# Kernel tuning notes

Hardware: AMD Instinct MI355X
Metric: run time of the kernel (lower is better)

Reference implementation:

```python
import jax, jax.numpy as jnp
import numpy as np

D = 128
N_SRC = 50000
N_DST = 50000
E = 640000
NEG_SLOPE = 0.01  # torch LeakyReLU default


def _lrelu(x):
    return jax.nn.leaky_relu(x, NEG_SLOPE)


def setup_inputs() -> dict:
    key = jax.random.key(0)
    ks = jax.random.split(key, 12)
    s = 1.0 / np.sqrt(D)
    return {
        "feat_src": jax.random.normal(ks[0], (N_SRC, D), jnp.float32),
        "feat_dst": jax.random.normal(ks[1], (N_DST, D), jnp.float32),
        "src_idx": jax.random.randint(ks[2], (E,), 0, N_SRC, jnp.int32),
        "dst_idx": jax.random.randint(ks[3], (E,), 0, N_DST, jnp.int32),
        "W_src": jax.random.uniform(ks[4], (D, D), jnp.float32, -s, s),
        "b_src": jnp.zeros((D,), jnp.float32),
        "W_dst": jax.random.uniform(ks[5], (D, D), jnp.float32, -s, s),
        "b_dst": jnp.zeros((D,), jnp.float32),
        "W_a1": jax.random.uniform(ks[6], (D, D), jnp.float32, -s, s),
        "b_a1": jnp.zeros((D,), jnp.float32),
        "W_a2": jax.random.uniform(ks[7], (D, 1), jnp.float32, -s, s),
        "b_a2": jnp.zeros((1,), jnp.float32),
        "W_out": jax.random.uniform(ks[8], (D, D), jnp.float32, -s, s),
        "b_out": jnp.zeros((D,), jnp.float32),
    }


def reference(feat_src, feat_dst, src_idx, dst_idx,
              W_src, b_src, W_dst, b_dst,
              W_a1, b_a1, W_a2, b_a2, W_out, b_out):
    n_dst = feat_dst.shape[0]
    # node projections (dropout is identity in eval mode)
    hs = feat_src @ W_src + b_src            # [n_src, d]
    hd = feat_dst @ W_dst + b_dst            # [n_dst, d]
    # u_add_v: per-edge feature
    e = hs[src_idx] + hd[dst_idx]            # [E, d]
    # attention MLP: LeakyReLU -> Linear -> LeakyReLU -> Linear(d->1)
    s = _lrelu(_lrelu(e) @ W_a1 + b_a1) @ W_a2 + b_a2  # [E, 1]
    s = s[:, 0]
    # edge softmax grouped by destination node (numerically stable)
    m = jax.ops.segment_max(s, dst_idx, num_segments=n_dst)
    ex = jnp.exp(s - m[dst_idx])
    denom = jax.ops.segment_sum(ex, dst_idx, num_segments=n_dst)
    alpha = ex / denom[dst_idx]              # [E]
    # scale messages and scatter-sum to dst nodes
    n_f = jax.ops.segment_sum(alpha[:, None] * e, dst_idx, num_segments=n_dst)
    return _lrelu(n_f @ W_out + b_out)       # [n_dst, d]
```

## Files before the change

kernel.cpp:

```cpp
#include <hip/hip_runtime.h>
#include <math.h>

#define DD 128
#define NEG 0.01f
#define SCHUNK 4096

typedef __attribute__((ext_vector_type(8))) _Float16 half8;
typedef __attribute__((ext_vector_type(4))) float f32x4;

__device__ __forceinline__ float lrelu(float x){ return x > 0.f ? x : NEG * x; }

__device__ __forceinline__ unsigned short h2u(_Float16 h){
    union { _Float16 h; unsigned short u; } v; v.h = h; return v.u;
}
__device__ __forceinline__ _Float16 u2h(unsigned short u){
    union { unsigned short u; _Float16 h; } v; v.u = u; return v.h;
}

__device__ __forceinline__ half8 h8max(half8 x, half8 y){
#if __has_builtin(__builtin_elementwise_max)
    return __builtin_elementwise_max(x, y);
#else
    half8 r;
    #pragma unroll
    for (int i = 0; i < 8; i++) r[i] = x[i] > y[i] ? x[i] : y[i];
    return r;
#endif
}

__global__ void hist_pack(const int* dst, int* deg, int E, int nhist,
                          const float* Wa1, const float* Wsrc,
                          const float* Wdst, const float* Wout,
                          unsigned short* wpack){
    const int bid = blockIdx.x;
    if (bid < nhist){
        int i = bid * 256 + threadIdx.x;
        if (i < E) atomicAdd(&deg[dst[i]], 1);
    } else {
        int i = (bid - nhist) * 256 + threadIdx.x;
        if (i >= 4 * 16384) return;
        int seg = i >> 14, t = i & 16383;
        int j = t & 7, lane = (t >> 3) & 63, nt = (t >> 9) & 7, kc = t >> 12;
        int k = kc * 32 + (lane >> 4) * 8 + j;
        int n = nt * 16 + (lane & 15);
        const float* W = (seg == 0) ? Wa1 : (seg == 1) ? Wsrc : (seg == 2) ? Wdst : Wout;
        wpack[i] = h2u((_Float16)W[k * DD + n]);
    }
}

__global__ __launch_bounds__(1024) void scan1(const int* deg, int* part, int n){
    __shared__ int wsum[16];
    const int tid = threadIdx.x;
    const int lane = tid & 63, wid = tid >> 6;
    int i4 = blockIdx.x * SCHUNK + tid * 4;
    int4 v = make_int4(0, 0, 0, 0);
    if (i4 + 3 < n) v = *(const int4*)(deg + i4);
    else {
        if (i4 + 0 < n) v.x = deg[i4 + 0];
        if (i4 + 1 < n) v.y = deg[i4 + 1];
        if (i4 + 2 < n) v.z = deg[i4 + 2];
        if (i4 + 3 < n) v.w = deg[i4 + 3];
    }
    int t = v.x + v.y + v.z + v.w;
    #pragma unroll
    for (int off = 1; off < 64; off <<= 1) t += __shfl_xor(t, off, 64);
    if (lane == 0) wsum[wid] = t;
    __syncthreads();
    if (tid == 0){
        int s = 0;
        #pragma unroll
        for (int j = 0; j < 16; j++) s += wsum[j];
        part[blockIdx.x] = s;
    }
}

__global__ __launch_bounds__(1024) void scan2(const int* deg, const int* part,
        int* row_off, int* cursor, int n, int nchunks){
    __shared__ int wsum[16];
    const int tid = threadIdx.x;
    const int lane = tid & 63, wid = tid >> 6;
    const int b = blockIdx.x;
    int carry = 0;
    for (int j = 0; j < b; j++) carry += part[j];
    int i4 = b * SCHUNK + tid * 4;
    int4 v = make_int4(0, 0, 0, 0);
    if (i4 + 3 < n) v = *(const int4*)(deg + i4);
    else {
        if (i4 + 0 < n) v.x = deg[i4 + 0];
        if (i4 + 1 < n) v.y = deg[i4 + 1];
        if (i4 + 2 < n) v.z = deg[i4 + 2];
        if (i4 + 3 < n) v.w = deg[i4 + 3];
    }
    int tsum = v.x + v.y + v.z + v.w;
    int x = tsum;
    #pragma unroll
    for (int off = 1; off < 64; off <<= 1){
        int t = __shfl_up(x, off, 64);
        if (lane >= off) x += t;
    }
    if (lane == 63) wsum[wid] = x;
    __syncthreads();
    int wprefix = 0;
    #pragma unroll
    for (int j = 0; j < 16; j++) if (j < wid) wprefix += wsum[j];
    int excl = carry + wprefix + (x - tsum);
    if (i4 + 3 < n){
        int4 o;
        o.x = excl; o.y = excl + v.x; o.z = o.y + v.y; o.w = o.z + v.z;
        *(int4*)(row_off + i4) = o;
        *(int4*)(cursor + i4) = o;
    } else {
        int a = excl;
        if (i4 + 0 < n){ row_off[i4 + 0] = a; cursor[i4 + 0] = a; a += v.x; }
        if (i4 + 1 < n){ row_off[i4 + 1] = a; cursor[i4 + 1] = a; a += v.y; }
        if (i4 + 2 < n){ row_off[i4 + 2] = a; cursor[i4 + 2] = a; a += v.z; }
        if (i4 + 3 < n){ row_off[i4 + 3] = a; cursor[i4 + 3] = a; }
    }
    if (b == 0 && tid == 0){
        int tot = 0;
        for (int j = 0; j < nchunks; j++) tot += part[j];
        row_off[n] = tot;
    }
}

__global__ void scatter_pairs(const int* src, const int* dst, int* cursor,
                              int2* pairs, int* s_srcs, int E){
    int i = blockIdx.x * blockDim.x + threadIdx.x;
    if (i < E){
        int d = dst[i];
        int s = src[i];
        int pos = atomicAdd(&cursor[d], 1);
        pairs[pos] = make_int2(s, d);
        s_srcs[pos] = s;
    }
}

__global__ __launch_bounds__(256) void lin2_mfma(
        const float* X1, const unsigned short* W1, const float* b1,
        unsigned short* Yb1, int n1, int g1,
        const float* X2, const unsigned short* W2, const float* b2,
        unsigned short* Yb2, int n2){
    __shared__ unsigned short sB[16384];
    const int tid = threadIdx.x;
    const int second = (blockIdx.x >= g1);
    const float* X = second ? X2 : X1;
    const unsigned short* W = second ? W2 : W1;
    const float* b = second ? b2 : b1;
    unsigned short* Yb = second ? Yb2 : Yb1;
    const int nrows = second ? n2 : n1;
    const int bidx = second ? (blockIdx.x - g1) : blockIdx.x;
    {
        const uint4* g = (const uint4*)W;
        uint4* l = (uint4*)sB;
        #pragma unroll
        for (int t = 0; t < 8; t++) l[tid + 256 * t] = g[tid + 256 * t];
    }
    const int wave = tid >> 6, lane = tid & 63;
    const int qd = lane >> 4, ln16 = lane & 15;
    const int row0 = bidx * 128 + wave * 32;
    int r0 = row0 + ln16;       if (r0 >= nrows) r0 = nrows - 1;
    int r1 = row0 + 16 + ln16;  if (r1 >= nrows) r1 = nrows - 1;
    f32x4 acc[2][8];
    #pragma unroll
    for (int rt = 0; rt < 2; rt++)
        #pragma unroll
        for (int nt = 0; nt < 8; nt++)
            acc[rt][nt] = (f32x4){0.f, 0.f, 0.f, 0.f};
    __syncthreads();
    #pragma unroll
    for (int kc = 0; kc < 4; kc++){
        const int koff = kc * 32 + qd * 8;
        half8 a[2];
        const float* px[2] = {X + (size_t)r0 * DD + koff, X + (size_t)r1 * DD + koff};
        #pragma unroll
        for (int rt = 0; rt < 2; rt++){
            float4 v0 = *(const float4*)(px[rt]);
            float4 v1 = *(const float4*)(px[rt] + 4);
            a[rt][0] = (_Float16)v0.x; a[rt][1] = (_Float16)v0.y;
            a[rt][2] = (_Float16)v0.z; a[rt][3] = (_Float16)v0.w;
            a[rt][4] = (_Float16)v1.x; a[rt][5] = (_Float16)v1.y;
            a[rt][6] = (_Float16)v1.z; a[rt][7] = (_Float16)v1.w;
        }
        #pragma unroll
        for (int nt = 0; nt < 8; nt++){
            const int fi = (((kc << 3) + nt) << 6 | lane) << 3;
            half8 bw = *(const half8*)&sB[fi];
            acc[0][nt] = __builtin_amdgcn_mfma_f32_16x16x32_f16(a[0], bw, acc[0][nt], 0, 0, 0);
            acc[1][nt] = __builtin_amdgcn_mfma_f32_16x16x32_f16(a[1], bw, acc[1][nt], 0, 0, 0);
        }
    }
    #pragma unroll
    for (int nt = 0; nt < 8; nt++){
        const int col = nt * 16 + ln16;
        const float bv = b[col];
        #pragma unroll
        for (int rt = 0; rt < 2; rt++){
            #pragma unroll
            for (int r = 0; r < 4; r++){
                int row = row0 + rt * 16 + qd * 4 + r;
                if (row < nrows){
                    float y = acc[rt][nt][r] + bv;
                    Yb[(size_t)row * DD + col] = h2u((_Float16)y);
                }
            }
        }
    }
}

__global__ __launch_bounds__(256) void lin_mfma(const float* X,
        const unsigned short* W, const float* b, float* Y, int nrows){
    __shared__ unsigned short sB[16384];
    const int tid = threadIdx.x;
    {
        const uint4* g = (const uint4*)W;
        uint4* l = (uint4*)sB;
        #pragma unroll
        for (int t = 0; t < 8; t++) l[tid + 256 * t] = g[tid + 256 * t];
    }
    const int wave = tid >> 6, lane = tid & 63;
    const int qd = lane >> 4, ln16 = lane & 15;
    const int row0 = blockIdx.x * 128 + wave * 32;
    int r0 = row0 + ln16;       if (r0 >= nrows) r0 = nrows - 1;
    int r1 = row0 + 16 + ln16;  if (r1 >= nrows) r1 = nrows - 1;
    f32x4 acc[2][8];
    #pragma unroll
    for (int rt = 0; rt < 2; rt++)
        #pragma unroll
        for (int nt = 0; nt < 8; nt++)
            acc[rt][nt] = (f32x4){0.f, 0.f, 0.f, 0.f};
    __syncthreads();
    #pragma unroll
    for (int kc = 0; kc < 4; kc++){
        const int koff = kc * 32 + qd * 8;
        half8 a[2];
        const float* px[2] = {X + (size_t)r0 * DD + koff, X + (size_t)r1 * DD + koff};
        #pragma unroll
        for (int rt = 0; rt < 2; rt++){
            float4 v0 = *(const float4*)(px[rt]);
            float4 v1 = *(const float4*)(px[rt] + 4);
            a[rt][0] = (_Float16)v0.x; a[rt][1] = (_Float16)v0.y;
            a[rt][2] = (_Float16)v0.z; a[rt][3] = (_Float16)v0.w;
            a[rt][4] = (_Float16)v1.x; a[rt][5] = (_Float16)v1.y;
            a[rt][6] = (_Float16)v1.z; a[rt][7] = (_Float16)v1.w;
        }
        #pragma unroll
        for (int nt = 0; nt < 8; nt++){
            const int fi = (((kc << 3) + nt) << 6 | lane) << 3;
            half8 bw = *(const half8*)&sB[fi];
            acc[0][nt] = __builtin_amdgcn_mfma_f32_16x16x32_f16(a[0], bw, acc[0][nt], 0, 0, 0);
            acc[1][nt] = __builtin_amdgcn_mfma_f32_16x16x32_f16(a[1], bw, acc[1][nt], 0, 0, 0);
        }
    }
    #pragma unroll
    for (int nt = 0; nt < 8; nt++){
        const int col = nt * 16 + ln16;
        const float bv = b[col];
        #pragma unroll
        for (int rt = 0; rt < 2; rt++){
            #pragma unroll
            for (int r = 0; r < 4; r++){
                int row = row0 + rt * 16 + qd * 4 + r;
                if (row < nrows){
                    float y = acc[rt][nt][r] + bv;
                    Y[(size_t)row * DD + col] = lrelu(y);
                }
            }
        }
    }
}

__device__ __forceinline__ half8 make_afrag(const unsigned short* ph, const unsigned short* pd){
    half8 a = *(const half8*)ph;
    half8 b = *(const half8*)pd;
    half8 s = a + b;
    return h8max(s, s * (_Float16)NEG);
}

__global__ __launch_bounds__(512) void edge_score_mfma(
        const unsigned short* hs_h, const unsigned short* hd_h,
        const int2* pairs,
        const unsigned short* wa1p, const float* ba1,
        const float* Wa2, const float* ba2,
        float* s_w, int E){
    __shared__ unsigned short sB[16384];
    const int tid = threadIdx.x;
    {
        const uint4* g = (const uint4*)wa1p;
        uint4* l = (uint4*)sB;
        #pragma unroll
        for (int t = 0; t < 4; t++) l[tid + 512 * t] = g[tid + 512 * t];
    }
    const int wave = tid >> 6, lane = tid & 63;
    const int qd = lane >> 4, ln16 = lane & 15;
    const int e0 = blockIdx.x * 256 + wave * 32;
    float b1v[8], w2v[8];
    #pragma unroll
    for (int nt = 0; nt < 8; nt++){
        b1v[nt] = ba1[nt * 16 + ln16];
        w2v[nt] = Wa2[nt * 16 + ln16];
    }
    const float b2 = ba2[0];
    __syncthreads();
    for (int rt = 0; rt < 2; rt++){
        int eid = e0 + rt * 16 + ln16;
        if (eid >= E) eid = E - 1;
        const int2 pp = pairs[eid];
        f32x4 acc[8];
        #pragma unroll
        for (int nt = 0; nt < 8; nt++)
            acc[nt] = (f32x4){b1v[nt], b1v[nt], b1v[nt], b1v[nt]};
        #pragma unroll
        for (int kc = 0; kc < 4; kc++){
            const int koff = kc * 32 + qd * 8;
            half8 af = make_afrag(hs_h + (size_t)pp.x * DD + koff,
                                  hd_h + (size_t)pp.y * DD + koff);
            #pragma unroll
            for (int nt = 0; nt < 8; nt++){
                half8 bf = *(const half8*)&sB[(((kc << 3) + nt) << 6 | lane) << 3];
                acc[nt] = __builtin_amdgcn_mfma_f32_16x16x32_f16(af, bf, acc[nt], 0, 0, 0);
            }
        }
        float p[4] = {0.f, 0.f, 0.f, 0.f};
        #pragma unroll
        for (int nt = 0; nt < 8; nt++)
            #pragma unroll
            for (int r = 0; r < 4; r++){
                float z = acc[nt][r];
                z = fmaxf(z, NEG * z);
                p[r] += z * w2v[nt];
            }
        #pragma unroll
        for (int r = 0; r < 4; r++){
            float v = p[r];
            #pragma unroll
            for (int off = 1; off < 16; off <<= 1) v += __shfl_xor(v, off, 64);
            p[r] = __expf(v + b2);
        }
        if (ln16 == 0){
            int row = e0 + rt * 16 + qd * 4;
            #pragma unroll
            for (int r = 0; r < 4; r++)
                if (row + r < E) s_w[row + r] = p[r];
        }
    }
}

__global__ __launch_bounds__(256) void agg_softmax(const unsigned short* hs_h,
        const unsigned short* hd_h, const int* row_off, const int* s_srcs,
        const float* s_w, float* nf, int n_dst){
    const int w = (blockIdx.x * blockDim.x + threadIdx.x) >> 6;
    const int lane = threadIdx.x & 63;
    if (w >= n_dst) return;
    const int beg = row_off[w], end = row_off[w + 1];
    float2 acc = make_float2(0.f, 0.f);
    float sa = 0.f;
    int e = beg;
    for (; e + 7 < end; e += 8){
        float wv[8]; int sv[8]; ushort2 uv[8];
        #pragma unroll
        for (int j = 0; j < 8; j++){ wv[j] = s_w[e + j]; sv[j] = s_srcs[e + j]; }
        #pragma unroll
        for (int j = 0; j < 8; j++)
            uv[j] = *(const ushort2*)(hs_h + (size_t)sv[j] * DD + lane * 2);
        #pragma unroll
        for (int j = 0; j < 8; j++){
            acc.x += wv[j] * (float)u2h(uv[j].x);
            acc.y += wv[j] * (float)u2h(uv[j].y);
            sa += wv[j];
        }
    }
    for (; e < end; e++){
        float w0 = s_w[e];
        int s0 = s_srcs[e];
        ushort2 u0 = *(const ushort2*)(hs_h + (size_t)s0 * DD + lane * 2);
        acc.x += w0 * (float)u2h(u0.x);
        acc.y += w0 * (float)u2h(u0.y);
        sa += w0;
    }
    const float inv = (end > beg) ? 1.f / sa : 0.f;
    ushort2 hu = *(const ushort2*)(hd_h + (size_t)w * DD + lane * 2);
    const float hx = (end > beg) ? (float)u2h(hu.x) : 0.f;
    const float hy = (end > beg) ? (float)u2h(hu.y) : 0.f;
    float2 out;
    out.x = acc.x * inv + hx;
    out.y = acc.y * inv + hy;
    *(float2*)(nf + (size_t)w * DD + lane * 2) = out;
}

extern "C" void kernel_launch(void* const* d_in, const int* in_sizes, int n_in,
                              void* d_out, int out_size, void* d_ws, size_t ws_size,
                              hipStream_t stream){
    const float* feat_src = (const float*)d_in[0];
    const float* feat_dst = (const float*)d_in[1];
    const int*   src_idx  = (const int*)d_in[2];
    const int*   dst_idx  = (const int*)d_in[3];
    const float* W_src = (const float*)d_in[4];
    const float* b_src = (const float*)d_in[5];
    const float* W_dst = (const float*)d_in[6];
    const float* b_dst = (const float*)d_in[7];
    const float* W_a1  = (const float*)d_in[8];
    const float* b_a1  = (const float*)d_in[9];
    const float* W_a2  = (const float*)d_in[10];
    const float* b_a2  = (const float*)d_in[11];
    const float* W_out = (const float*)d_in[12];
    const float* b_out = (const float*)d_in[13];
    const int n_src = in_sizes[0] / DD;
    const int n_dst = in_sizes[1] / DD;
    const int E = in_sizes[2];
    const int nchunks = (n_dst + SCHUNK - 1) / SCHUNK;

    char* p = (char*)d_ws;
    unsigned short* hs_h = (unsigned short*)p;  p += (size_t)n_src * DD * 2;
    unsigned short* hd_h = (unsigned short*)p;  p += (size_t)n_dst * DD * 2;
    unsigned short* wpack = (unsigned short*)p; p += 4 * 16384 * 2;
    float* s_w = (float*)p;                     p += (size_t)E * 4;
    int2* pairs = (int2*)p;                     p += (size_t)E * 8;
    int* s_srcs = (int*)p;                      p += (size_t)E * 4;
    int* deg = (int*)p;                         p += (size_t)n_dst * 4;
    int* cursor = (int*)p;                      p += (size_t)n_dst * 4;
    int* part = (int*)p;                        p += 64 * 4;
    int* row_off = (int*)p;                     p += ((size_t)n_dst + 1) * 4;
    float* nf = (float*)d_out;

    const unsigned short* wa1p = wpack;
    const unsigned short* wsrc = wpack + 1 * 16384;
    const unsigned short* wdst = wpack + 2 * 16384;
    const unsigned short* wout = wpack + 3 * 16384;

    hipMemsetAsync(deg, 0, (size_t)n_dst * 4, stream);
    const int nhist = (E + 255) / 256;
    const int npack = (4 * 16384 + 255) / 256;
    hist_pack<<<nhist + npack, 256, 0, stream>>>(dst_idx, deg, E, nhist,
                                                 W_a1, W_src, W_dst, W_out, wpack);
    scan1<<<nchunks, 1024, 0, stream>>>(deg, part, n_dst);
    scan2<<<nchunks, 1024, 0, stream>>>(deg, part, row_off, cursor, n_dst, nchunks);
    scatter_pairs<<<(E + 255) / 256, 256, 0, stream>>>(src_idx, dst_idx, cursor,
                                                       pairs, s_srcs, E);
    const int g1 = (n_src + 127) / 128;
    const int g2 = (n_dst + 127) / 128;
    lin2_mfma<<<g1 + g2, 256, 0, stream>>>(feat_src, wsrc, b_src, hs_h, n_src, g1,
                                           feat_dst, wdst, b_dst, hd_h, n_dst);
    edge_score_mfma<<<(E + 255) / 256, 512, 0, stream>>>(hs_h, hd_h, pairs, wa1p, b_a1,
                                                         W_a2, b_a2, s_w, E);
    agg_softmax<<<((size_t)n_dst * 64 + 255) / 256, 256, 0, stream>>>(hs_h, hd_h, row_off,
                                                                      s_srcs, s_w, nf, n_dst);
    lin_mfma<<<g2, 256, 0, stream>>>(nf, wout, b_out, nf, n_dst);
}
```

Measured before the change: 300.7 us.

## Prefetch second edge tile in score kernel, split agg wave across two edges

The edge score kernel now loads the feature rows for its second 16-edge tile before running the first tile's epilogue, so gather latency overlaps with compute. It also adds an occupancy hint to launch bounds. The aggregation kernel splits each wave into two half-waves that handle alternate edges with 8-byte loads, then combines them with a cross-half shuffle. It reads source indices from the pairs array, so the separate s_srcs buffer and its scatter writes are removed. In exchange, register pressure rises and the index reads are strided 8-byte loads.

```diff
diff --git a/kernel.cpp b/kernel.cpp
--- a/kernel.cpp
+++ b/kernel.cpp
@@ -124,14 +124,13 @@
 }
 
 __global__ void scatter_pairs(const int* src, const int* dst, int* cursor,
-                              int2* pairs, int* s_srcs, int E){
+                              int2* pairs, int E){
     int i = blockIdx.x * blockDim.x + threadIdx.x;
     if (i < E){
         int d = dst[i];
         int s = src[i];
         int pos = atomicAdd(&cursor[d], 1);
         pairs[pos] = make_int2(s, d);
-        s_srcs[pos] = s;
     }
 }
 
@@ -269,14 +268,38 @@
     }
 }
 
-__device__ __forceinline__ half8 make_afrag(const unsigned short* ph, const unsigned short* pd){
-    half8 a = *(const half8*)ph;
-    half8 b = *(const half8*)pd;
+__device__ __forceinline__ half8 afrag_from(half8 a, half8 b){
     half8 s = a + b;
     return h8max(s, s * (_Float16)NEG);
 }
 
-__global__ __launch_bounds__(512) void edge_score_mfma(
+__device__ __forceinline__ void score_epilogue(const f32x4* acc, const float* w2v,
+        float b2, int e0rt, int qd, int ln16, float* s_w, int E){
+    float p[4] = {0.f, 0.f, 0.f, 0.f};
+    #pragma unroll
+    for (int nt = 0; nt < 8; nt++)
+        #pragma unroll
+        for (int r = 0; r < 4; r++){
+            float z = acc[nt][r];
+            z = fmaxf(z, NEG * z);
+            p[r] += z * w2v[nt];
+        }
+    #pragma unroll
+    for (int r = 0; r < 4; r++){
+        float v = p[r];
+        #pragma unroll
+        for (int off = 1; off < 16; off <<= 1) v += __shfl_xor(v, off, 64);
+        p[r] = __expf(v + b2);
+    }
+    if (ln16 == 0){
+        int row = e0rt + qd * 4;
+        #pragma unroll
+        for (int r = 0; r < 4; r++)
+            if (row + r < E) s_w[row + r] = p[r];
+    }
+}
+
+__global__ __launch_bounds__(512, 4) void edge_score_mfma(
         const unsigned short* hs_h, const unsigned short* hd_h,
         const int2* pairs,
         const unsigned short* wa1p, const float* ba1,
@@ -301,90 +324,114 @@
     }
     const float b2 = ba2[0];
     __syncthreads();
-    for (int rt = 0; rt < 2; rt++){
-        int eid = e0 + rt * 16 + ln16;
-        if (eid >= E) eid = E - 1;
-        const int2 pp = pairs[eid];
-        f32x4 acc[8];
-        #pragma unroll
-        for (int nt = 0; nt < 8; nt++)
-            acc[nt] = (f32x4){b1v[nt], b1v[nt], b1v[nt], b1v[nt]};
-        #pragma unroll
-        for (int kc = 0; kc < 4; kc++){
-            const int koff = kc * 32 + qd * 8;
-            half8 af = make_afrag(hs_h + (size_t)pp.x * DD + koff,
-                                  hd_h + (size_t)pp.y * DD + koff);
-            #pragma unroll
-            for (int nt = 0; nt < 8; nt++){
-                half8 bf = *(const half8*)&sB[(((kc << 3) + nt) << 6 | lane) << 3];
-                acc[nt] = __builtin_amdgcn_mfma_f32_16x16x32_f16(af, bf, acc[nt], 0, 0, 0);
-            }
-        }
-        float p[4] = {0.f, 0.f, 0.f, 0.f};
-        #pragma unroll
-        for (int nt = 0; nt < 8; nt++)
-            #pragma unroll
-            for (int r = 0; r < 4; r++){
-                float z = acc[nt][r];
-                z = fmaxf(z, NEG * z);
-                p[r] += z * w2v[nt];
-            }
-        #pragma unroll
-        for (int r = 0; r < 4; r++){
-            float v = p[r];
-            #pragma unroll
-            for (int off = 1; off < 16; off <<= 1) v += __shfl_xor(v, off, 64);
-            p[r] = __expf(v + b2);
-        }
-        if (ln16 == 0){
-            int row = e0 + rt * 16 + qd * 4;
-            #pragma unroll
-            for (int r = 0; r < 4; r++)
-                if (row + r < E) s_w[row + r] = p[r];
-        }
-    }
+
+    int eid0 = e0 + ln16;       if (eid0 >= E) eid0 = E - 1;
+    int eid1 = e0 + 16 + ln16;  if (eid1 >= E) eid1 = E - 1;
+    const int2 pp0 = pairs[eid0];
+    const int2 pp1 = pairs[eid1];
+    const unsigned short* ps0 = hs_h + (size_t)pp0.x * DD;
+    const unsigned short* pd0 = hd_h + (size_t)pp0.y * DD;
+    const unsigned short* ps1 = hs_h + (size_t)pp1.x * DD;
+    const unsigned short* pd1 = hd_h + (size_t)pp1.y * DD;
+
+    f32x4 acc0[8];
+    #pragma unroll
+    for (int nt = 0; nt < 8; nt++)
+        acc0[nt] = (f32x4){b1v[nt], b1v[nt], b1v[nt], b1v[nt]};
+    #pragma unroll
+    for (int kc = 0; kc < 4; kc++){
+        const int koff = kc * 32 + qd * 8;
+        half8 af = afrag_from(*(const half8*)(ps0 + koff), *(const half8*)(pd0 + koff));
+        #pragma unroll
+        for (int nt = 0; nt < 8; nt++){
+            half8 bf = *(const half8*)&sB[(((kc << 3) + nt) << 6 | lane) << 3];
+            acc0[nt] = __builtin_amdgcn_mfma_f32_16x16x32_f16(af, bf, acc0[nt], 0, 0, 0);
+        }
+    }
+    half8 ra[4], rb[4];
+    #pragma unroll
+    for (int kc = 0; kc < 4; kc++){
+        const int koff = kc * 32 + qd * 8;
+        ra[kc] = *(const half8*)(ps1 + koff);
+        rb[kc] = *(const half8*)(pd1 + koff);
+    }
+    score_epilogue(acc0, w2v, b2, e0, qd, ln16, s_w, E);
+    f32x4 acc1[8];
+    #pragma unroll
+    for (int nt = 0; nt < 8; nt++)
+        acc1[nt] = (f32x4){b1v[nt], b1v[nt], b1v[nt], b1v[nt]};
+    #pragma unroll
+    for (int kc = 0; kc < 4; kc++){
+        half8 af = afrag_from(ra[kc], rb[kc]);
+        #pragma unroll
+        for (int nt = 0; nt < 8; nt++){
+            half8 bf = *(const half8*)&sB[(((kc << 3) + nt) << 6 | lane) << 3];
+            acc1[nt] = __builtin_amdgcn_mfma_f32_16x16x32_f16(af, bf, acc1[nt], 0, 0, 0);
+        }
+    }
+    score_epilogue(acc1, w2v, b2, e0 + 16, qd, ln16, s_w, E);
 }
 
 __global__ __launch_bounds__(256) void agg_softmax(const unsigned short* hs_h,
-        const unsigned short* hd_h, const int* row_off, const int* s_srcs,
+        const unsigned short* hd_h, const int* row_off, const int2* pairs,
         const float* s_w, float* nf, int n_dst){
     const int w = (blockIdx.x * blockDim.x + threadIdx.x) >> 6;
     const int lane = threadIdx.x & 63;
     if (w >= n_dst) return;
     const int beg = row_off[w], end = row_off[w + 1];
-    float2 acc = make_float2(0.f, 0.f);
+    const int hf = lane >> 5, l32 = lane & 31;
+    float4 acc = make_float4(0.f, 0.f, 0.f, 0.f);
     float sa = 0.f;
     int e = beg;
     for (; e + 7 < end; e += 8){
-        float wv[8]; int sv[8]; ushort2 uv[8];
-        #pragma unroll
-        for (int j = 0; j < 8; j++){ wv[j] = s_w[e + j]; sv[j] = s_srcs[e + j]; }
-        #pragma unroll
-        for (int j = 0; j < 8; j++)
-            uv[j] = *(const ushort2*)(hs_h + (size_t)sv[j] * DD + lane * 2);
-        #pragma unroll
-        for (int j = 0; j < 8; j++){
+        int rows[4]; float wv[4]; ushort4 uv[4];
+        #pragma unroll
+        for (int j = 0; j < 4; j++){
+            int ee = e + 2 * j + hf;
+            rows[j] = pairs[ee].x;
+            wv[j] = s_w[ee];
+        }
+        #pragma unroll
+        for (int j = 0; j < 4; j++)
+            uv[j] = *(const ushort4*)(hs_h + (size_t)rows[j] * DD + l32 * 4);
+        #pragma unroll
+        for (int j = 0; j < 4; j++){
             acc.x += wv[j] * (float)u2h(uv[j].x);
             acc.y += wv[j] * (float)u2h(uv[j].y);
+            acc.z += wv[j] * (float)u2h(uv[j].z);
+            acc.w += wv[j] * (float)u2h(uv[j].w);
             sa += wv[j];
         }
     }
-    for (; e < end; e++){
-        float w0 = s_w[e];
-        int s0 = s_srcs[e];
-        ushort2 u0 = *(const ushort2*)(hs_h + (size_t)s0 * DD + lane * 2);
-        acc.x += w0 * (float)u2h(u0.x);
-        acc.y += w0 * (float)u2h(u0.y);
-        sa += w0;
-    }
+    for (; e < end; e += 2){
+        int ee = e + hf;
+        float wv = 0.f;
+        int row;
+        if (ee < end){ row = pairs[ee].x; wv = s_w[ee]; }
+        else row = pairs[end - 1].x;
+        ushort4 uv = *(const ushort4*)(hs_h + (size_t)row * DD + l32 * 4);
+        acc.x += wv * (float)u2h(uv.x);
+        acc.y += wv * (float)u2h(uv.y);
+        acc.z += wv * (float)u2h(uv.z);
+        acc.w += wv * (float)u2h(uv.w);
+        sa += wv;
+    }
+    acc.x += __shfl_xor(acc.x, 32, 64);
+    acc.y += __shfl_xor(acc.y, 32, 64);
+    acc.z += __shfl_xor(acc.z, 32, 64);
+    acc.w += __shfl_xor(acc.w, 32, 64);
+    sa    += __shfl_xor(sa, 32, 64);
     const float inv = (end > beg) ? 1.f / sa : 0.f;
-    ushort2 hu = *(const ushort2*)(hd_h + (size_t)w * DD + lane * 2);
-    const float hx = (end > beg) ? (float)u2h(hu.x) : 0.f;
-    const float hy = (end > beg) ? (float)u2h(hu.y) : 0.f;
-    float2 out;
-    out.x = acc.x * inv + hx;
-    out.y = acc.y * inv + hy;
-    *(float2*)(nf + (size_t)w * DD + lane * 2) = out;
+    if (hf == 0){
+        ushort4 hu = *(const ushort4*)(hd_h + (size_t)w * DD + l32 * 4);
+        const float gx = (end > beg) ? 1.f : 0.f;
+        float4 out;
+        out.x = acc.x * inv + gx * (float)u2h(hu.x);
+        out.y = acc.y * inv + gx * (float)u2h(hu.y);
+        out.z = acc.z * inv + gx * (float)u2h(hu.z);
+        out.w = acc.w * inv + gx * (float)u2h(hu.w);
+        *(float4*)(nf + (size_t)w * DD + l32 * 4) = out;
+    }
 }
 
 extern "C" void kernel_launch(void* const* d_in, const int* in_sizes, int n_in,
@@ -415,7 +462,6 @@
     unsigned short* wpack = (unsigned short*)p; p += 4 * 16384 * 2;
     float* s_w = (float*)p;                     p += (size_t)E * 4;
     int2* pairs = (int2*)p;                     p += (size_t)E * 8;
-    int* s_srcs = (int*)p;                      p += (size_t)E * 4;
     int* deg = (int*)p;                         p += (size_t)n_dst * 4;
     int* cursor = (int*)p;                      p += (size_t)n_dst * 4;
     int* part = (int*)p;                        p += 64 * 4;
@@ -435,7 +481,7 @@
     scan1<<<nchunks, 1024, 0, stream>>>(deg, part, n_dst);
     scan2<<<nchunks, 1024, 0, stream>>>(deg, part, row_off, cursor, n_dst, nchunks);
     scatter_pairs<<<(E + 255) / 256, 256, 0, stream>>>(src_idx, dst_idx, cursor,
-                                                       pairs, s_srcs, E);
+                                                       pairs, E);
     const int g1 = (n_src + 127) / 128;
     const int g2 = (n_dst + 127) / 128;
     lin2_mfma<<<g1 + g2, 256, 0, stream>>>(feat_src, wsrc, b_src, hs_h, n_src, g1,
@@ -443,6 +489,6 @@
     edge_score_mfma<<<(E + 255) / 256, 512, 0, stream>>>(hs_h, hd_h, pairs, wa1p, b_a1,
                                                          W_a2, b_a2, s_w, E);
     agg_softmax<<<((size_t)n_dst * 64 + 255) / 256, 256, 0, stream>>>(hs_h, hd_h, row_off,
-                                                                      s_srcs, s_w, nf, n_dst);
+                                                                      pairs, s_w, nf, n_dst);
     lin_mfma<<<g2, 256, 0, stream>>>(nf, wout, b_out, nf, n_dst);
 }
```

Result: no change. 298.6 us (-0.7%).
